# Performance work log

Measured on AMD Instinct MI355X. Metric: run time of the kernel, lower is better.

The kernel has to match this reference:

```python
import jax, jax.numpy as jnp
import numpy as np

N = 30000      # nodes
E = 480000     # edges
K = 32         # subgraph size per node
P = 16384      # contrastive pairs
IN = 1024      # in_dim
H = 512        # hidden
Z = 128        # latent (zdim)
BN = 8         # batch_num
DB = 16        # dec_batch_dim
DEC0 = Z + DB  # decoder input dim after concat with batch embedding


def _ln(x):
    m = jnp.mean(x, axis=-1, keepdims=True)
    v = jnp.var(x, axis=-1, keepdims=True)
    return (x - m) * jax.lax.rsqrt(v + 1e-5)


def _gin(x, src, dst, W, b, norm=True, act=True):
    # GIN aggregation (eps=0): (1+eps)*x + sum_{j in N(i)} x_j, then MLP/linear
    agg = jax.ops.segment_sum(x[src], dst, num_segments=N)
    h = (x + agg) @ W + b
    if norm:
        h = _ln(h)
    if act:
        h = jax.nn.relu(h)
    return h


def _encode(x, src, dst, W0, b0, W1, b1):
    h = _gin(x, src, dst, W0, b0, norm=True, act=True)
    return _gin(h, src, dst, W1, b1, norm=True, act=True)  # last_norm=True


def _decode(z, src, dst, W0, b0, W1, b1):
    h = _gin(z, src, dst, W0, b0, norm=True, act=True)
    return _gin(h, src, dst, W1, b1, norm=False, act=False)  # last_norm=False


def setup_inputs() -> dict:
    key = jax.random.key(0)
    ks = jax.random.split(key, 24)
    s = 0.02
    inp = {
        "x": jax.random.normal(ks[0], (N, IN), jnp.float32),
        "x_shf": jax.random.normal(ks[1], (N, IN), jnp.float32),
        "batch_labels": jax.random.uniform(ks[2], (N, BN), jnp.float32),
        "enc_W0": s * jax.random.normal(ks[3], (IN, H), jnp.float32),
        "enc_b0": jnp.zeros((H,), jnp.float32),
        "enc_W1": s * jax.random.normal(ks[4], (H, Z), jnp.float32),
        "enc_b1": jnp.zeros((Z,), jnp.float32),
        "dec_W0": s * jax.random.normal(ks[5], (DEC0, H), jnp.float32),
        "dec_b0": jnp.zeros((H,), jnp.float32),
        "dec_W1": s * jax.random.normal(ks[6], (H, IN), jnp.float32),
        "dec_b1": jnp.zeros((IN,), jnp.float32),
        "be_W0": s * jax.random.normal(ks[7], (BN, (BN + DB) // 2), jnp.float32),
        "be_b0": jnp.zeros(((BN + DB) // 2,), jnp.float32),
        "be_W1": s * jax.random.normal(ks[8], ((BN + DB) // 2, DB), jnp.float32),
        "be_b1": jnp.zeros((DB,), jnp.float32),
        "bd_W0": s * jax.random.normal(ks[9], (Z, 64), jnp.float32),
        "bd_b0": jnp.zeros((64,), jnp.float32),
        "bd_W1": s * jax.random.normal(ks[10], (64, BN), jnp.float32),
        "bd_b1": jnp.zeros((BN,), jnp.float32),
        "bil_W": s * jax.random.normal(ks[11], (Z, Z), jnp.float32),
        "edge_index": jax.random.randint(ks[12], (2, E), 0, N, jnp.int32),
        "sub_node_idx": jax.random.randint(ks[13], (N, K), 0, N, jnp.int32),
        "positive_ind": jax.random.randint(ks[14], (P,), 0, N, jnp.int32),
        "negative_ind": jax.random.randint(ks[15], (P,), 0, N, jnp.int32),
    }
    return inp


def reference(x, x_shf, batch_labels, enc_W0, enc_b0, enc_W1, enc_b1,
              dec_W0, dec_b0, dec_W1, dec_b1, be_W0, be_b0, be_W1, be_b1,
              bd_W0, bd_b0, bd_W1, bd_b1, bil_W,
              edge_index, sub_node_idx, positive_ind, negative_ind):
    src, dst = edge_index[0], edge_index[1]

    # encoder + subgraph mean pooling (global_mean_pool over fixed-size subgraphs)
    z_node = _encode(x, src, dst, enc_W0, enc_b0, enc_W1, enc_b1)        # [N, Z]
    z_sub = jnp.mean(z_node[sub_node_idx], axis=1)                        # [N, Z]
    z_node_shf = _encode(x_shf, src, dst, enc_W0, enc_b0, enc_W1, enc_b1)
    z_sub_shf = jnp.mean(z_node_shf[sub_node_idx], axis=1)                # [N, Z]

    # batch encoder (MLP, no norm)
    batch_emb = jax.nn.relu(batch_labels @ be_W0 + be_b0) @ be_W1 + be_b1  # [N, DB]

    # bilinear contrastive discriminator
    zp = z_sub[positive_ind]                                              # [P, Z]
    logits_pos = jnp.einsum('pd,de,pe->p', zp, bil_W, z_sub_shf[positive_ind])
    logits_neg = jnp.einsum('pd,de,pe->p', zp, bil_W, z_sub_shf[negative_ind])

    # batch discriminator (MLP)
    logits_batch = jax.nn.relu(z_sub @ bd_W0 + bd_b0) @ bd_W1 + bd_b1     # [N, BN]

    # decoder over node graph with batch embedding concatenated
    z_node_batch = jnp.concatenate([z_node, batch_emb], axis=1)           # [N, Z+DB]
    recon = _decode(z_node_batch, src, dst, dec_W0, dec_b0, dec_W1, dec_b1)  # [N, IN]

    return (z_sub, z_sub_shf, recon, logits_pos, logits_neg, logits_batch)
```

## Files before the change

### kernel.cpp

```cpp
#include <hip/hip_runtime.h>
#include <hip/hip_bf16.h>

#define N_NODES 30000
#define E_EDGES 480000
#define KSUB 32
#define NPAIR 16384

typedef __hip_bfloat16 bf16;
typedef __bf16 bf16x8 __attribute__((ext_vector_type(8)));
typedef float floatx4 __attribute__((ext_vector_type(4)));

static __device__ __forceinline__ unsigned short f2bu(float f) {
    unsigned int u = __float_as_uint(f);
    unsigned int r = (u + 0x7fffu + ((u >> 16) & 1u)) >> 16;
    return (unsigned short)r;
}
static __device__ __forceinline__ float blo(unsigned int u) { return __uint_as_float(u << 16); }
static __device__ __forceinline__ float bhi(unsigned int u) { return __uint_as_float(u & 0xffff0000u); }
static __device__ __forceinline__ unsigned int pk2(float a, float b) {
    return (unsigned int)f2bu(a) | ((unsigned int)f2bu(b) << 16);
}

typedef __attribute__((address_space(1))) const void ga_void;
typedef __attribute__((address_space(3))) void lds_void;
static __device__ __forceinline__ void async16(const void* g, void* l) {
    __builtin_amdgcn_global_load_lds((ga_void*)g, (lds_void*)l, 16, 0, 0);
}

__global__ void transpose_pad(const float* __restrict__ W, int K, int Nd,
                              unsigned short* __restrict__ Wt, int Kpad) {
    int t = blockIdx.x * 256 + threadIdx.x;
    if (t >= Nd * Kpad) return;
    int n = t / Kpad, k = t - n * Kpad;
    Wt[t] = (k < K) ? f2bu(W[(size_t)k * Nd + n]) : (unsigned short)0;
}

__global__ void edge_hist(const int* __restrict__ dst, int* __restrict__ deg) {
    int e = blockIdx.x * 256 + threadIdx.x;
    if (e < E_EDGES) atomicAdd(&deg[dst[e]], 1);
}

__global__ void scan_kernel(const int* __restrict__ deg, int N,
                            int* __restrict__ row_start, int* __restrict__ cursor) {
    __shared__ int sh[1024];
    int t = threadIdx.x;
    int chunk = (N + 1023) >> 10;
    int lo = t * chunk;
    int hi = lo + chunk; if (hi > N) hi = N;
    if (lo > N) lo = N;
    int s = 0;
    for (int i = lo; i < hi; i++) s += deg[i];
    sh[t] = s;
    __syncthreads();
    for (int off = 1; off < 1024; off <<= 1) {
        int v = (t >= off) ? sh[t - off] : 0;
        __syncthreads();
        sh[t] += v;
        __syncthreads();
    }
    int run = (t == 0) ? 0 : sh[t - 1];
    for (int i = lo; i < hi; i++) {
        row_start[i] = run; cursor[i] = run; run += deg[i];
    }
    if (t == 1023) row_start[N] = run;
}

__global__ void edge_scatter(const int* __restrict__ src, const int* __restrict__ dst,
                             int* __restrict__ cursor, int* __restrict__ csr_src) {
    int e = blockIdx.x * 256 + threadIdx.x;
    if (e < E_EDGES) {
        int p = atomicAdd(&cursor[dst[e]], 1);
        if (p >= 0 && p < E_EDGES) csr_src[p] = src[e];
    }
}

template <int D, int DOUT, int DO_LN>
__global__ void csr_agg_ln_h(const unsigned short* __restrict__ X,
                             const int* __restrict__ row_start,
                             const int* __restrict__ csr_src,
                             const float* __restrict__ bias,
                             unsigned short* __restrict__ Y,
                             int addCenter, int doRelu) {
    constexpr int VE = (D % 512 == 0) ? 8 : 2;
    constexpr int R = (D + 64 * VE - 1) / (64 * VE);
    static_assert(VE == 2 || R == 1, "VE8 path assumes single round");
    static_assert(!DO_LN || (D % (64 * VE) == 0), "LN path needs full lanes");
    constexpr int U = D / 2;
    constexpr int UO = DOUT / 2;
    static_assert(D % 2 == 0 && DOUT % 2 == 0, "even dims");

    int node = blockIdx.x * 4 + (threadIdx.x >> 6);
    if (node >= N_NODES) return;
    int lane = threadIdx.x & 63;

    float acc[R][VE];
#pragma unroll
    for (int r = 0; r < R; r++)
#pragma unroll
        for (int i = 0; i < VE; i++) acc[r][i] = 0.0f;

    int s0 = row_start[node], s1 = row_start[node + 1];
    if (s0 < 0) s0 = 0;
    if (s1 > E_EDGES) s1 = E_EDGES;

    if constexpr (VE == 8) {
        auto add_u4 = [&](uint4 u) {
            acc[0][0] += blo(u.x); acc[0][1] += bhi(u.x);
            acc[0][2] += blo(u.y); acc[0][3] += bhi(u.y);
            acc[0][4] += blo(u.z); acc[0][5] += bhi(u.z);
            acc[0][6] += blo(u.w); acc[0][7] += bhi(u.w);
        };
        if (addCenter)
            add_u4(*reinterpret_cast<const uint4*>(X + (size_t)node * D + lane * 8));
        for (int j0 = s0; j0 < s1; j0 += 64) {
            int cnt = s1 - j0; if (cnt > 64) cnt = 64;
            int myi = (lane < cnt) ? csr_src[j0 + lane] : 0;
            int t = 0;
            for (; t + 8 <= cnt; t += 8) {
                uint4 raw[8];
#pragma unroll
                for (int g = 0; g < 8; g++) {
                    int s = __shfl(myi, t + g);
                    if ((unsigned)s >= (unsigned)N_NODES) s = 0;
                    raw[g] = *reinterpret_cast<const uint4*>(X + (size_t)s * D + lane * 8);
                }
#pragma unroll
                for (int g = 0; g < 8; g++) add_u4(raw[g]);
            }
            for (; t < cnt; t++) {
                int s = __shfl(myi, t);
                if ((unsigned)s >= (unsigned)N_NODES) s = 0;
                add_u4(*reinterpret_cast<const uint4*>(X + (size_t)s * D + lane * 8));
            }
        }
        if (bias) {
            const float4* bp = reinterpret_cast<const float4*>(bias + lane * 8);
            float4 b0 = bp[0], b1 = bp[1];
            acc[0][0] += b0.x; acc[0][1] += b0.y; acc[0][2] += b0.z; acc[0][3] += b0.w;
            acc[0][4] += b1.x; acc[0][5] += b1.y; acc[0][6] += b1.z; acc[0][7] += b1.w;
        }
    } else {
        auto add_u = [&](int r, unsigned int u) { acc[r][0] += blo(u); acc[r][1] += bhi(u); };
        if (addCenter) {
#pragma unroll
            for (int r = 0; r < R; r++) {
                int unit = r * 64 + lane;
                if (unit < U)
                    add_u(r, *reinterpret_cast<const unsigned int*>(X + (size_t)node * D + unit * 2));
            }
        }
        for (int j0 = s0; j0 < s1; j0 += 64) {
            int cnt = s1 - j0; if (cnt > 64) cnt = 64;
            int myi = (lane < cnt) ? csr_src[j0 + lane] : 0;
            int t = 0;
            for (; t + 8 <= cnt; t += 8) {
                unsigned int raw[8][R];
#pragma unroll
                for (int g = 0; g < 8; g++) {
                    int s = __shfl(myi, t + g);
                    if ((unsigned)s >= (unsigned)N_NODES) s = 0;
#pragma unroll
                    for (int r = 0; r < R; r++) {
                        int unit = r * 64 + lane;
                        raw[g][r] = (unit < U)
                            ? *reinterpret_cast<const unsigned int*>(X + (size_t)s * D + unit * 2)
                            : 0u;
                    }
                }
#pragma unroll
                for (int g = 0; g < 8; g++)
#pragma unroll
                    for (int r = 0; r < R; r++) add_u(r, raw[g][r]);
            }
            for (; t < cnt; t++) {
                int s = __shfl(myi, t);
                if ((unsigned)s >= (unsigned)N_NODES) s = 0;
#pragma unroll
                for (int r = 0; r < R; r++) {
                    int unit = r * 64 + lane;
                    if (unit < U)
                        add_u(r, *reinterpret_cast<const unsigned int*>(X + (size_t)s * D + unit * 2));
                }
            }
        }
        if (bias) {
#pragma unroll
            for (int r = 0; r < R; r++) {
                int unit = r * 64 + lane;
                if (unit < U) { acc[r][0] += bias[unit * 2]; acc[r][1] += bias[unit * 2 + 1]; }
            }
        }
    }

    if constexpr (DO_LN) {
        float s = 0.0f;
#pragma unroll
        for (int r = 0; r < R; r++)
#pragma unroll
            for (int i = 0; i < VE; i++) s += acc[r][i];
        for (int o = 32; o; o >>= 1) s += __shfl_xor(s, o);
        float mean = s * (1.0f / (float)D);
        float q = 0.0f;
#pragma unroll
        for (int r = 0; r < R; r++)
#pragma unroll
            for (int i = 0; i < VE; i++) { float d = acc[r][i] - mean; q += d * d; }
        for (int o = 32; o; o >>= 1) q += __shfl_xor(q, o);
        float rs_ = rsqrtf(q * (1.0f / (float)D) + 1e-5f);
#pragma unroll
        for (int r = 0; r < R; r++)
#pragma unroll
            for (int i = 0; i < VE; i++) acc[r][i] = (acc[r][i] - mean) * rs_;
    }

    if (doRelu) {
#pragma unroll
        for (int r = 0; r < R; r++)
#pragma unroll
            for (int i = 0; i < VE; i++) if (acc[r][i] < 0.0f) acc[r][i] = 0.0f;
    }

    if constexpr (VE == 8) {
        uint4 o = make_uint4(pk2(acc[0][0], acc[0][1]), pk2(acc[0][2], acc[0][3]),
                             pk2(acc[0][4], acc[0][5]), pk2(acc[0][6], acc[0][7]));
        *reinterpret_cast<uint4*>(Y + (size_t)node * DOUT + lane * 8) = o;
    } else {
        constexpr int RO = (UO + 63) / 64;
#pragma unroll
        for (int r = 0; r < RO; r++) {
            int unit = r * 64 + lane;
            if (unit < UO) {
                unsigned int v = 0u;
                if (r < R && unit < U) v = pk2(acc[r][0], acc[r][1]);
                *reinterpret_cast<unsigned int*>(Y + (size_t)node * DOUT + unit * 2) = v;
            }
        }
    }
}

__global__ void ln_relu_h512(const unsigned short* __restrict__ Yin,
                             const float* __restrict__ bias,
                             unsigned short* __restrict__ Out) {
    int row = blockIdx.x * 4 + (threadIdx.x >> 6);
    if (row >= N_NODES) return;
    int lane = threadIdx.x & 63;
    uint4 u = *reinterpret_cast<const uint4*>(Yin + (size_t)row * 512 + lane * 8);
    const float4* bp = reinterpret_cast<const float4*>(bias + lane * 8);
    float4 b0 = bp[0], b1 = bp[1];
    float v[8];
    v[0] = blo(u.x) + b0.x; v[1] = bhi(u.x) + b0.y;
    v[2] = blo(u.y) + b0.z; v[3] = bhi(u.y) + b0.w;
    v[4] = blo(u.z) + b1.x; v[5] = bhi(u.z) + b1.y;
    v[6] = blo(u.w) + b1.z; v[7] = bhi(u.w) + b1.w;
    float s = 0.0f;
#pragma unroll
    for (int i = 0; i < 8; i++) s += v[i];
    for (int o = 32; o; o >>= 1) s += __shfl_xor(s, o);
    float mean = s * (1.0f / 512.0f);
    float q = 0.0f;
#pragma unroll
    for (int i = 0; i < 8; i++) { float d = v[i] - mean; q += d * d; }
    for (int o = 32; o; o >>= 1) q += __shfl_xor(q, o);
    float rs = rsqrtf(q * (1.0f / 512.0f) + 1e-5f);
#pragma unroll
    for (int i = 0; i < 8; i++) {
        float o = (v[i] - mean) * rs;
        v[i] = o > 0.0f ? o : 0.0f;
    }
    uint4 o = make_uint4(pk2(v[0], v[1]), pk2(v[2], v[3]), pk2(v[4], v[5]), pk2(v[6], v[7]));
    *reinterpret_cast<uint4*>(Out + (size_t)row * 512 + lane * 8) = o;
}

template <int ABF, int CBF, int BLKN>
__global__ __launch_bounds__(BLKN * 2, 2) void gemm_bt(
    const void* __restrict__ A_, int lda, const unsigned short* __restrict__ Bt,
    int M, int K, void* __restrict__ C_, int ldc, const float* __restrict__ bias,
    int nbn) {
    constexpr int THREADS = BLKN * 2;
    constexpr int NW = THREADS / 64;
    constexpr int WNC = BLKN / 64;
    constexpr int ASTR = ABF ? 64 : 72;
    __shared__ __align__(16) unsigned short As[128 * ASTR];
    __shared__ __align__(16) unsigned short Bs[BLKN * 64];

    int lid = blockIdx.x;
    int bmlow = lid & 7;
    int t2 = lid >> 3;
    int bmh = t2 / nbn;
    int bn = t2 - bmh * nbn;
    int bm = bmh * 8 + bmlow;
    if (bm * 128 >= M) return;

    const int t = threadIdx.x;
    const int lane = t & 63;
    const int wave = t >> 6;
    const int wm = wave / WNC, wn = wave % WNC;
    const int quad = lane >> 4, m16 = lane & 15;

    floatx4 acc[4][4];
#pragma unroll
    for (int i = 0; i < 4; i++)
#pragma unroll
        for (int j = 0; j < 4; j++)
#pragma unroll
            for (int r = 0; r < 4; r++) acc[i][j][r] = 0.0f;

    union Pk { unsigned short h[8]; uint4 v; };
    const int l8 = lane >> 3;
    const int gseg = (lane & 7) ^ l8;

    for (int k0 = 0; k0 < K; k0 += 64) {
        if constexpr (ABF) {
            constexpr int ACALLS = 128 / (NW * 8);
#pragma unroll
            for (int i = 0; i < ACALLS; i++) {
                int rb = (i * NW + wave) * 8;
                const unsigned short* gp = (const unsigned short*)A_ +
                    (size_t)(bm * 128 + rb + l8) * lda + k0 + gseg * 8;
                async16(gp, &As[rb * 64]);
            }
        } else {
            constexpr int GR = 1024 / THREADS;
#pragma unroll
            for (int i = 0; i < GR; i++) {
                int q = i * THREADS + t;
                int r = q >> 3, g = q & 7;
                int grow = bm * 128 + r;
                uint4 val = make_uint4(0u, 0u, 0u, 0u);
                if (grow < M) {
                    const float* ap = (const float*)A_ + (size_t)grow * lda + k0 + g * 8;
                    float4 f0 = *reinterpret_cast<const float4*>(ap);
                    float4 f1 = *reinterpret_cast<const float4*>(ap + 4);
                    Pk pk;
                    pk.h[0] = f2bu(f0.x); pk.h[1] = f2bu(f0.y);
                    pk.h[2] = f2bu(f0.z); pk.h[3] = f2bu(f0.w);
                    pk.h[4] = f2bu(f1.x); pk.h[5] = f2bu(f1.y);
                    pk.h[6] = f2bu(f1.z); pk.h[7] = f2bu(f1.w);
                    val = pk.v;
                }
                *reinterpret_cast<uint4*>(&As[r * 72 + g * 8]) = val;
            }
        }
        constexpr int BCALLS = BLKN / (NW * 8);
#pragma unroll
        for (int i = 0; i < BCALLS; i++) {
            int rb = (i * NW + wave) * 8;
            const unsigned short* gp = Bt + (size_t)(bn * BLKN + rb + l8) * K + k0 + gseg * 8;
            async16(gp, &Bs[rb * 64]);
        }
        __syncthreads();
#pragma unroll
        for (int kk = 0; kk < 2; kk++) {
            bf16x8 af[4], bfr[4];
#pragma unroll
            for (int i = 0; i < 4; i++) {
                int r = wm * 64 + i * 16 + m16;
                int off;
                if constexpr (ABF) off = r * 64 + (((kk * 4 + quad) ^ (r & 7)) * 8);
                else off = r * 72 + (kk * 4 + quad) * 8;
                af[i] = *reinterpret_cast<const bf16x8*>(&As[off]);
            }
#pragma unroll
            for (int j = 0; j < 4; j++) {
                int r = wn * 64 + j * 16 + m16;
                bfr[j] = *reinterpret_cast<const bf16x8*>(&Bs[r * 64 + (((kk * 4 + quad) ^ (r & 7)) * 8)]);
            }
#pragma unroll
            for (int i = 0; i < 4; i++)
#pragma unroll
                for (int j = 0; j < 4; j++)
                    acc[i][j] = __builtin_amdgcn_mfma_f32_16x16x32_bf16(af[i], bfr[j], acc[i][j], 0, 0, 0);
        }
        __syncthreads();
    }
#pragma unroll
    for (int i = 0; i < 4; i++) {
        int r0 = bm * 128 + wm * 64 + i * 16 + quad * 4;
#pragma unroll
        for (int j = 0; j < 4; j++) {
            int c = bn * BLKN + wn * 64 + j * 16 + m16;
            float bia = bias ? bias[c] : 0.0f;
#pragma unroll
            for (int r = 0; r < 4; r++) {
                int row = r0 + r;
                if (row < M) {
                    float val = acc[i][j][r] + bia;
                    if constexpr (CBF)
                        ((unsigned short*)C_)[(size_t)row * ldc + c] = f2bu(val);
                    else
                        ((float*)C_)[(size_t)row * ldc + c] = val;
                }
            }
        }
    }
}

__global__ void pool_kernel_h(const unsigned short* __restrict__ zn, const int* __restrict__ idx,
                              float* __restrict__ out) {
    int i = blockIdx.x * 4 + (threadIdx.x >> 6);
    if (i >= N_NODES) return;
    int lane = threadIdx.x & 63;
    int myi = (lane < KSUB) ? idx[i * KSUB + lane] : 0;
    float ax = 0.0f, ay = 0.0f;
#pragma unroll
    for (int t = 0; t < KSUB; t++) {
        int s = __shfl(myi, t);
        if ((unsigned)s >= (unsigned)N_NODES) s = 0;
        unsigned int u = *reinterpret_cast<const unsigned int*>(zn + (size_t)s * 128 + lane * 2);
        ax += blo(u); ay += bhi(u);
    }
    *reinterpret_cast<float2*>(out + (size_t)i * 128 + lane * 2) =
        make_float2(ax * (1.0f / KSUB), ay * (1.0f / KSUB));
}

__global__ void batch_emb_kernel(const float* __restrict__ bl, const float* __restrict__ W0,
                                 const float* __restrict__ b0, const float* __restrict__ W1,
                                 const float* __restrict__ b1, float* __restrict__ out) {
    int i = blockIdx.x * 256 + threadIdx.x;
    if (i >= N_NODES) return;
    float in[8];
#pragma unroll
    for (int d = 0; d < 8; d++) in[d] = bl[(size_t)i * 8 + d];
    float h[12];
#pragma unroll
    for (int j = 0; j < 12; j++) {
        float a = b0[j];
#pragma unroll
        for (int d = 0; d < 8; d++) a += in[d] * W0[d * 12 + j];
        h[j] = a > 0.0f ? a : 0.0f;
    }
#pragma unroll
    for (int j = 0; j < 16; j++) {
        float a = b1[j];
#pragma unroll
        for (int k = 0; k < 12; k++) a += h[k] * W1[k * 16 + j];
        out[(size_t)i * 16 + j] = a;
    }
}

__global__ void concat_kernel_h(const unsigned short* __restrict__ zn,
                                const float* __restrict__ be,
                                unsigned short* __restrict__ znb) {
    int i = blockIdx.x;
    int t = threadIdx.x;
    if (t < 128) znb[(size_t)i * 144 + t] = zn[(size_t)i * 128 + t];
    else if (t < 144) znb[(size_t)i * 144 + t] = f2bu(be[(size_t)i * 16 + (t - 128)]);
}

__global__ void bilinear_dot(const float* __restrict__ U, const float* __restrict__ z_shf,
                             const int* __restrict__ pos, const int* __restrict__ neg,
                             float* __restrict__ out_pos, float* __restrict__ out_neg) {
    int p = blockIdx.x * 4 + (threadIdx.x >> 6);
    if (p >= NPAIR) return;
    int lane = threadIdx.x & 63;
    int ip = pos[p], in_ = neg[p];
    if ((unsigned)ip >= (unsigned)N_NODES) ip = 0;
    if ((unsigned)in_ >= (unsigned)N_NODES) in_ = 0;
    float2 u = *reinterpret_cast<const float2*>(U + (size_t)ip * 128 + lane * 2);
    float2 zp = *reinterpret_cast<const float2*>(z_shf + (size_t)ip * 128 + lane * 2);
    float2 zn = *reinterpret_cast<const float2*>(z_shf + (size_t)in_ * 128 + lane * 2);
    float vp = u.x * zp.x + u.y * zp.y;
    float vn = u.x * zn.x + u.y * zn.y;
    for (int o = 32; o; o >>= 1) { vp += __shfl_xor(vp, o); vn += __shfl_xor(vn, o); }
    if (lane == 0) { out_pos[p] = vp; out_neg[p] = vn; }
}

__global__ void bd_kernel(const float* __restrict__ z_sub, const float* __restrict__ W0,
                          const float* __restrict__ b0, const float* __restrict__ W1,
                          const float* __restrict__ b1, float* __restrict__ out) {
    __shared__ float zsh[4][128];
    __shared__ float hsh[4][64];
    int w = threadIdx.x >> 6, lane = threadIdx.x & 63;
    int node = blockIdx.x * 4 + w;
    zsh[w][lane] = z_sub[(size_t)node * 128 + lane];
    zsh[w][64 + lane] = z_sub[(size_t)node * 128 + 64 + lane];
    __syncthreads();
    float h = b0[lane];
    for (int d = 0; d < 128; d++) h += zsh[w][d] * W0[d * 64 + lane];
    if (h < 0.0f) h = 0.0f;
    hsh[w][lane] = h;
    __syncthreads();
    if (lane < 8) {
        float o = b1[lane];
        for (int l = 0; l < 64; l++) o += hsh[w][l] * W1[l * 8 + lane];
        out[(size_t)node * 8 + lane] = o;
    }
}

extern "C" void kernel_launch(void* const* d_in, const int* in_sizes, int n_in,
                              void* d_out, int out_size, void* d_ws, size_t ws_size,
                              hipStream_t stream) {
    const float* x = (const float*)d_in[0];
    const float* x_shf = (const float*)d_in[1];
    const float* blab = (const float*)d_in[2];
    const float* encW0 = (const float*)d_in[3];
    const float* encb0 = (const float*)d_in[4];
    const float* encW1 = (const float*)d_in[5];
    const float* encb1 = (const float*)d_in[6];
    const float* decW0 = (const float*)d_in[7];
    const float* decb0 = (const float*)d_in[8];
    const float* decW1 = (const float*)d_in[9];
    const float* decb1 = (const float*)d_in[10];
    const float* beW0 = (const float*)d_in[11];
    const float* beb0 = (const float*)d_in[12];
    const float* beW1 = (const float*)d_in[13];
    const float* beb1 = (const float*)d_in[14];
    const float* bdW0 = (const float*)d_in[15];
    const float* bdb0 = (const float*)d_in[16];
    const float* bdW1 = (const float*)d_in[17];
    const float* bdb1 = (const float*)d_in[18];
    const float* bilW = (const float*)d_in[19];
    const int* eidx = (const int*)d_in[20];
    const int* subidx = (const int*)d_in[21];
    const int* posi = (const int*)d_in[22];
    const int* negi = (const int*)d_in[23];
    float* out = (float*)d_out;

    char* ws = (char*)d_ws;
    size_t off = 0;
    auto alloc = [&](size_t bytes) -> void* {
        void* p = ws + off;
        off += (bytes + 255) & ~(size_t)255;
        return p;
    };
    unsigned short* encW0t = (unsigned short*)alloc((size_t)512 * 1024 * 2);
    unsigned short* encW1t = (unsigned short*)alloc((size_t)128 * 512 * 2);
    unsigned short* decW0t = (unsigned short*)alloc((size_t)512 * 192 * 2);
    unsigned short* decW1t = (unsigned short*)alloc((size_t)1024 * 512 * 2);
    unsigned short* bilWt = (unsigned short*)alloc((size_t)128 * 128 * 2);
    int* deg = (int*)alloc((size_t)N_NODES * 4);
    int* row_start = (int*)alloc((size_t)(N_NODES + 1) * 4);
    int* cursor = (int*)alloc((size_t)N_NODES * 4);
    int* csr_src = (int*)alloc((size_t)E_EDGES * 4);
    unsigned short* y0h = (unsigned short*)alloc((size_t)N_NODES * 512 * 2);
    unsigned short* agg0h = (unsigned short*)alloc((size_t)N_NODES * 512 * 2);
    unsigned short* y1h = (unsigned short*)alloc((size_t)N_NODES * 128 * 2);
    unsigned short* znh = (unsigned short*)alloc((size_t)N_NODES * 128 * 2);
    unsigned short* znsh = (unsigned short*)alloc((size_t)N_NODES * 128 * 2);
    unsigned short* znbh = (unsigned short*)alloc((size_t)N_NODES * 144 * 2);
    unsigned short* s1h = (unsigned short*)alloc((size_t)N_NODES * 192 * 2);
    float* bembf = (float*)alloc((size_t)N_NODES * 16 * 4);
    float* Ubil = (float*)alloc((size_t)N_NODES * 128 * 4);
    alloc(262144);
    if (off > ws_size) return;

    const int* e_src = eidx;
    const int* e_dst = eidx + E_EDGES;

    transpose_pad<<<(512 * 1024 + 255) / 256, 256, 0, stream>>>(encW0, 1024, 512, encW0t, 1024);
    transpose_pad<<<(128 * 512 + 255) / 256, 256, 0, stream>>>(encW1, 512, 128, encW1t, 512);
    transpose_pad<<<(512 * 192 + 255) / 256, 256, 0, stream>>>(decW0, 144, 512, decW0t, 192);
    transpose_pad<<<(1024 * 512 + 255) / 256, 256, 0, stream>>>(decW1, 512, 1024, decW1t, 512);
    transpose_pad<<<(128 * 128 + 255) / 256, 256, 0, stream>>>(bilW, 128, 128, bilWt, 128);

    hipMemsetAsync(deg, 0, (size_t)N_NODES * 4, stream);
    edge_hist<<<E_EDGES / 256, 256, 0, stream>>>(e_dst, deg);
    scan_kernel<<<1, 1024, 0, stream>>>(deg, N_NODES, row_start, cursor);
    edge_scatter<<<E_EDGES / 256, 256, 0, stream>>>(e_src, e_dst, cursor, csr_src);

    for (int pass = 0; pass < 2; pass++) {
        const float* xin = pass ? x_shf : x;
        unsigned short* zn = pass ? znsh : znh;
        float* zsub_out = out + (pass ? 3840000 : 0);
        gemm_bt<0, 1, 256><<<480, 512, 0, stream>>>(xin, 1024, encW0t, N_NODES, 1024, y0h, 512, nullptr, 2);
        csr_agg_ln_h<512, 512, 1><<<7500, 256, 0, stream>>>(y0h, row_start, csr_src, encb0, agg0h, 1, 1);
        gemm_bt<1, 1, 128><<<240, 256, 0, stream>>>(agg0h, 512, encW1t, N_NODES, 512, y1h, 128, nullptr, 1);
        csr_agg_ln_h<128, 128, 1><<<7500, 256, 0, stream>>>(y1h, row_start, csr_src, encb1, zn, 1, 1);
        pool_kernel_h<<<7500, 256, 0, stream>>>(zn, subidx, zsub_out);
    }

    batch_emb_kernel<<<(N_NODES + 255) / 256, 256, 0, stream>>>(blab, beW0, beb0, beW1, beb1, bembf);
    concat_kernel_h<<<30000, 192, 0, stream>>>(znh, bembf, znbh);

    csr_agg_ln_h<144, 192, 0><<<7500, 256, 0, stream>>>(znbh, row_start, csr_src, nullptr, s1h, 1, 0);
    gemm_bt<1, 1, 256><<<480, 512, 0, stream>>>(s1h, 192, decW0t, N_NODES, 192, y0h, 512, nullptr, 2);
    ln_relu_h512<<<7500, 256, 0, stream>>>(y0h, decb0, y0h);
    csr_agg_ln_h<512, 512, 0><<<7500, 256, 0, stream>>>(y0h, row_start, csr_src, nullptr, agg0h, 1, 0);
    gemm_bt<1, 0, 256><<<960, 512, 0, stream>>>(agg0h, 512, decW1t, N_NODES, 512, out + 7680000, 1024, decb1, 4);

    gemm_bt<0, 0, 128><<<240, 256, 0, stream>>>(out, 128, bilWt, N_NODES, 128, Ubil, 128, nullptr, 1);
    bilinear_dot<<<(NPAIR + 3) / 4, 256, 0, stream>>>(Ubil, out + 3840000, posi, negi,
                                                      out + 38400000, out + 38416384);
    bd_kernel<<<7500, 256, 0, stream>>>(out, bdW0, bdb0, bdW1, bdb1, out + 38432768);
}
```

Before: 1.060 ms.

## Batch both encoder passes, fuse concat into decoder aggregation, double-buffer gathers

Runs the original and shuffled encoder passes together: their outputs go into stacked 60000-row buffers so each aggregation, the second GEMM and the pooling launch once over both. The five weight transposes become a single kernel, and the concat kernel is removed by a dedicated decoder aggregation that reads z and the batch embedding directly. The D=512 gather loop is software-pipelined with two 8-row register buffers, the narrow path gathers 16 rows per batch, and launch bounds are added. The aim is to cut launch count, fill the GPU better, and keep more memory loads in flight, at the cost of higher register pressure and more complex indexing.

Measured after the change: 1.015 ms. 4.3% less time.

```diff
diff --git a/kernel.cpp b/kernel.cpp
--- a/kernel.cpp
+++ b/kernel.cpp
@@ -27,12 +27,22 @@
     __builtin_amdgcn_global_load_lds((ga_void*)g, (lds_void*)l, 16, 0, 0);
 }
 
-__global__ void transpose_pad(const float* __restrict__ W, int K, int Nd,
-                              unsigned short* __restrict__ Wt, int Kpad) {
+__global__ void transpose_all(const float* __restrict__ encW0, const float* __restrict__ encW1,
+                              const float* __restrict__ decW0, const float* __restrict__ decW1,
+                              const float* __restrict__ bilW,
+                              unsigned short* __restrict__ encW0t, unsigned short* __restrict__ encW1t,
+                              unsigned short* __restrict__ decW0t, unsigned short* __restrict__ decW1t,
+                              unsigned short* __restrict__ bilWt) {
     int t = blockIdx.x * 256 + threadIdx.x;
-    if (t >= Nd * Kpad) return;
-    int n = t / Kpad, k = t - n * Kpad;
-    Wt[t] = (k < K) ? f2bu(W[(size_t)k * Nd + n]) : (unsigned short)0;
+    const float* W; unsigned short* Wt; int K, Nd, Kpad, u;
+    if (t < 524288) { W = encW0; Wt = encW0t; K = 1024; Nd = 512; Kpad = 1024; u = t; }
+    else if (t < 589824) { W = encW1; Wt = encW1t; K = 512; Nd = 128; Kpad = 512; u = t - 524288; }
+    else if (t < 688128) { W = decW0; Wt = decW0t; K = 144; Nd = 512; Kpad = 192; u = t - 589824; }
+    else if (t < 1212416) { W = decW1; Wt = decW1t; K = 512; Nd = 1024; Kpad = 512; u = t - 688128; }
+    else if (t < 1228800) { W = bilW; Wt = bilWt; K = 128; Nd = 128; Kpad = 128; u = t - 1212416; }
+    else return;
+    int n = u / Kpad, k = u - n * Kpad;
+    Wt[u] = (k < K) ? f2bu(W[(size_t)k * Nd + n]) : (unsigned short)0;
 }
 
 __global__ void edge_hist(const int* __restrict__ dst, int* __restrict__ deg) {
@@ -75,23 +85,21 @@
 }
 
 template <int D, int DOUT, int DO_LN>
-__global__ void csr_agg_ln_h(const unsigned short* __restrict__ X,
-                             const int* __restrict__ row_start,
-                             const int* __restrict__ csr_src,
-                             const float* __restrict__ bias,
-                             unsigned short* __restrict__ Y,
-                             int addCenter, int doRelu) {
+__global__ __launch_bounds__(256, 4) void csr_agg_ln_h(
+    const unsigned short* __restrict__ Xa, const unsigned short* __restrict__ Xb, int nv,
+    const int* __restrict__ row_start, const int* __restrict__ csr_src,
+    const float* __restrict__ bias, unsigned short* __restrict__ Y,
+    int addCenter, int doRelu) {
     constexpr int VE = (D % 512 == 0) ? 8 : 2;
     constexpr int R = (D + 64 * VE - 1) / (64 * VE);
     static_assert(VE == 2 || R == 1, "VE8 path assumes single round");
-    static_assert(!DO_LN || (D % (64 * VE) == 0), "LN path needs full lanes");
-    constexpr int U = D / 2;
-    constexpr int UO = DOUT / 2;
-    static_assert(D % 2 == 0 && DOUT % 2 == 0, "even dims");
-
-    int node = blockIdx.x * 4 + (threadIdx.x >> 6);
-    if (node >= N_NODES) return;
+    static_assert(D % (64 * VE) == 0 && D == DOUT, "paths need exact divisibility");
+
+    int v = blockIdx.x * 4 + (threadIdx.x >> 6);
+    if (v >= nv) return;
     int lane = threadIdx.x & 63;
+    const unsigned short* X = (v < N_NODES) ? Xa : Xb;
+    int node = (v < N_NODES) ? v : v - N_NODES;
 
     float acc[R][VE];
 #pragma unroll
@@ -115,22 +123,32 @@
         for (int j0 = s0; j0 < s1; j0 += 64) {
             int cnt = s1 - j0; if (cnt > 64) cnt = 64;
             int myi = (lane < cnt) ? csr_src[j0 + lane] : 0;
-            int t = 0;
-            for (; t + 8 <= cnt; t += 8) {
-                uint4 raw[8];
+            uint4 rawA[8], rawB[8];
+            auto issue8 = [&](uint4 (&raw)[8], int tb) {
 #pragma unroll
                 for (int g = 0; g < 8; g++) {
-                    int s = __shfl(myi, t + g);
+                    int s = __shfl(myi, (tb + g) & 63);
                     if ((unsigned)s >= (unsigned)N_NODES) s = 0;
                     raw[g] = *reinterpret_cast<const uint4*>(X + (size_t)s * D + lane * 8);
                 }
-#pragma unroll
-                for (int g = 0; g < 8; g++) add_u4(raw[g]);
-            }
-            for (; t < cnt; t++) {
-                int s = __shfl(myi, t);
-                if ((unsigned)s >= (unsigned)N_NODES) s = 0;
-                add_u4(*reinterpret_cast<const uint4*>(X + (size_t)s * D + lane * 8));
+            };
+            auto consume8 = [&](uint4 (&raw)[8], int tb) {
+#pragma unroll
+                for (int g = 0; g < 8; g++)
+                    if (tb + g < cnt) add_u4(raw[g]);
+            };
+            issue8(rawA, 0);
+            int t = 0;
+            while (true) {
+                if (t + 8 < cnt) {
+                    issue8(rawB, t + 8);
+                    consume8(rawA, t);
+                    if (t + 16 < cnt) {
+                        issue8(rawA, t + 16);
+                        consume8(rawB, t + 8);
+                        t += 16;
+                    } else { consume8(rawB, t + 8); break; }
+                } else { consume8(rawA, t); break; }
             }
         }
         if (bias) {
@@ -143,51 +161,34 @@
         auto add_u = [&](int r, unsigned int u) { acc[r][0] += blo(u); acc[r][1] += bhi(u); };
         if (addCenter) {
 #pragma unroll
-            for (int r = 0; r < R; r++) {
-                int unit = r * 64 + lane;
-                if (unit < U)
-                    add_u(r, *reinterpret_cast<const unsigned int*>(X + (size_t)node * D + unit * 2));
-            }
+            for (int r = 0; r < R; r++)
+                add_u(r, *reinterpret_cast<const unsigned int*>(X + (size_t)node * D + (r * 64 + lane) * 2));
         }
         for (int j0 = s0; j0 < s1; j0 += 64) {
             int cnt = s1 - j0; if (cnt > 64) cnt = 64;
             int myi = (lane < cnt) ? csr_src[j0 + lane] : 0;
-            int t = 0;
-            for (; t + 8 <= cnt; t += 8) {
-                unsigned int raw[8][R];
-#pragma unroll
-                for (int g = 0; g < 8; g++) {
-                    int s = __shfl(myi, t + g);
+            for (int t = 0; t < cnt; t += 16) {
+                unsigned int raw[16][R];
+#pragma unroll
+                for (int g = 0; g < 16; g++) {
+                    int s = __shfl(myi, (t + g) & 63);
                     if ((unsigned)s >= (unsigned)N_NODES) s = 0;
 #pragma unroll
-                    for (int r = 0; r < R; r++) {
-                        int unit = r * 64 + lane;
-                        raw[g][r] = (unit < U)
-                            ? *reinterpret_cast<const unsigned int*>(X + (size_t)s * D + unit * 2)
-                            : 0u;
-                    }
+                    for (int r = 0; r < R; r++)
+                        raw[g][r] = *reinterpret_cast<const unsigned int*>(X + (size_t)s * D + (r * 64 + lane) * 2);
                 }
 #pragma unroll
-                for (int g = 0; g < 8; g++)
-#pragma unroll
-                    for (int r = 0; r < R; r++) add_u(r, raw[g][r]);
-            }
-            for (; t < cnt; t++) {
-                int s = __shfl(myi, t);
-                if ((unsigned)s >= (unsigned)N_NODES) s = 0;
-#pragma unroll
-                for (int r = 0; r < R; r++) {
-                    int unit = r * 64 + lane;
-                    if (unit < U)
-                        add_u(r, *reinterpret_cast<const unsigned int*>(X + (size_t)s * D + unit * 2));
-                }
+                for (int g = 0; g < 16; g++)
+                    if (t + g < cnt)
+#pragma unroll
+                        for (int r = 0; r < R; r++) add_u(r, raw[g][r]);
             }
         }
         if (bias) {
 #pragma unroll
             for (int r = 0; r < R; r++) {
                 int unit = r * 64 + lane;
-                if (unit < U) { acc[r][0] += bias[unit * 2]; acc[r][1] += bias[unit * 2 + 1]; }
+                acc[r][0] += bias[unit * 2]; acc[r][1] += bias[unit * 2 + 1];
             }
         }
     }
@@ -223,19 +224,64 @@
     if constexpr (VE == 8) {
         uint4 o = make_uint4(pk2(acc[0][0], acc[0][1]), pk2(acc[0][2], acc[0][3]),
                              pk2(acc[0][4], acc[0][5]), pk2(acc[0][6], acc[0][7]));
-        *reinterpret_cast<uint4*>(Y + (size_t)node * DOUT + lane * 8) = o;
+        *reinterpret_cast<uint4*>(Y + (size_t)v * DOUT + lane * 8) = o;
     } else {
-        constexpr int RO = (UO + 63) / 64;
-#pragma unroll
-        for (int r = 0; r < RO; r++) {
-            int unit = r * 64 + lane;
-            if (unit < UO) {
-                unsigned int v = 0u;
-                if (r < R && unit < U) v = pk2(acc[r][0], acc[r][1]);
-                *reinterpret_cast<unsigned int*>(Y + (size_t)node * DOUT + unit * 2) = v;
-            }
-        }
-    }
+#pragma unroll
+        for (int r = 0; r < R; r++)
+            *reinterpret_cast<unsigned int*>(Y + (size_t)v * DOUT + (r * 64 + lane) * 2) =
+                pk2(acc[r][0], acc[r][1]);
+    }
+}
+
+__global__ __launch_bounds__(256, 4) void csr_agg_dec(
+    const unsigned short* __restrict__ zn, const float* __restrict__ be,
+    const int* __restrict__ row_start, const int* __restrict__ csr_src,
+    unsigned short* __restrict__ Y) {
+    int node = blockIdx.x * 4 + (threadIdx.x >> 6);
+    if (node >= N_NODES) return;
+    int lane = threadIdx.x & 63;
+    float az0 = 0.0f, az1 = 0.0f, ab0 = 0.0f, ab1 = 0.0f;
+    {
+        unsigned int u = *reinterpret_cast<const unsigned int*>(zn + (size_t)node * 128 + lane * 2);
+        az0 += blo(u); az1 += bhi(u);
+        if (lane < 8) {
+            float2 b = *reinterpret_cast<const float2*>(be + (size_t)node * 16 + lane * 2);
+            ab0 += b.x; ab1 += b.y;
+        }
+    }
+    int s0 = row_start[node], s1 = row_start[node + 1];
+    if (s0 < 0) s0 = 0;
+    if (s1 > E_EDGES) s1 = E_EDGES;
+    for (int j0 = s0; j0 < s1; j0 += 64) {
+        int cnt = s1 - j0; if (cnt > 64) cnt = 64;
+        int myi = (lane < cnt) ? csr_src[j0 + lane] : 0;
+        for (int t = 0; t < cnt; t += 8) {
+            unsigned int rawZ[8]; float2 rawB[8];
+            int sv[8];
+#pragma unroll
+            for (int g = 0; g < 8; g++) {
+                int s = __shfl(myi, (t + g) & 63);
+                if ((unsigned)s >= (unsigned)N_NODES) s = 0;
+                sv[g] = s;
+                rawZ[g] = *reinterpret_cast<const unsigned int*>(zn + (size_t)s * 128 + lane * 2);
+            }
+            if (lane < 8) {
+#pragma unroll
+                for (int g = 0; g < 8; g++)
+                    rawB[g] = *reinterpret_cast<const float2*>(be + (size_t)sv[g] * 16 + lane * 2);
+            }
+#pragma unroll
+            for (int g = 0; g < 8; g++) {
+                if (t + g < cnt) {
+                    az0 += blo(rawZ[g]); az1 += bhi(rawZ[g]);
+                    if (lane < 8) { ab0 += rawB[g].x; ab1 += rawB[g].y; }
+                }
+            }
+        }
+    }
+    unsigned int* yr = reinterpret_cast<unsigned int*>(Y + (size_t)node * 192);
+    yr[lane] = pk2(az0, az1);
+    if (lane < 32) yr[64 + lane] = (lane < 8) ? pk2(ab0, ab1) : 0u;
 }
 
 __global__ void ln_relu_h512(const unsigned short* __restrict__ Yin,
@@ -397,20 +443,23 @@
 
 __global__ void pool_kernel_h(const unsigned short* __restrict__ zn, const int* __restrict__ idx,
                               float* __restrict__ out) {
-    int i = blockIdx.x * 4 + (threadIdx.x >> 6);
-    if (i >= N_NODES) return;
+    int v = blockIdx.x * 4 + (threadIdx.x >> 6);
+    if (v >= 2 * N_NODES) return;
     int lane = threadIdx.x & 63;
+    int pass = v >= N_NODES;
+    int i = pass ? v - N_NODES : v;
+    int roff = pass ? N_NODES : 0;
     int myi = (lane < KSUB) ? idx[i * KSUB + lane] : 0;
     float ax = 0.0f, ay = 0.0f;
 #pragma unroll
     for (int t = 0; t < KSUB; t++) {
         int s = __shfl(myi, t);
         if ((unsigned)s >= (unsigned)N_NODES) s = 0;
-        unsigned int u = *reinterpret_cast<const unsigned int*>(zn + (size_t)s * 128 + lane * 2);
+        unsigned int u = *reinterpret_cast<const unsigned int*>(zn + (size_t)(s + roff) * 128 + lane * 2);
         ax += blo(u); ay += bhi(u);
     }
-    *reinterpret_cast<float2*>(out + (size_t)i * 128 + lane * 2) =
-        make_float2(ax * (1.0f / KSUB), ay * (1.0f / KSUB));
+    float* op = out + (pass ? 3840000 : 0) + (size_t)i * 128 + lane * 2;
+    *reinterpret_cast<float2*>(op) = make_float2(ax * (1.0f / KSUB), ay * (1.0f / KSUB));
 }
 
 __global__ void batch_emb_kernel(const float* __restrict__ bl, const float* __restrict__ W0,
@@ -436,15 +485,6 @@
         for (int k = 0; k < 12; k++) a += h[k] * W1[k * 16 + j];
         out[(size_t)i * 16 + j] = a;
     }
-}
-
-__global__ void concat_kernel_h(const unsigned short* __restrict__ zn,
-                                const float* __restrict__ be,
-                                unsigned short* __restrict__ znb) {
-    int i = blockIdx.x;
-    int t = threadIdx.x;
-    if (t < 128) znb[(size_t)i * 144 + t] = zn[(size_t)i * 128 + t];
-    else if (t < 144) znb[(size_t)i * 144 + t] = f2bu(be[(size_t)i * 16 + (t - 128)]);
 }
 
 __global__ void bilinear_dot(const float* __restrict__ U, const float* __restrict__ z_shf,
@@ -532,12 +572,10 @@
     int* row_start = (int*)alloc((size_t)(N_NODES + 1) * 4);
     int* cursor = (int*)alloc((size_t)N_NODES * 4);
     int* csr_src = (int*)alloc((size_t)E_EDGES * 4);
-    unsigned short* y0h = (unsigned short*)alloc((size_t)N_NODES * 512 * 2);
-    unsigned short* agg0h = (unsigned short*)alloc((size_t)N_NODES * 512 * 2);
-    unsigned short* y1h = (unsigned short*)alloc((size_t)N_NODES * 128 * 2);
-    unsigned short* znh = (unsigned short*)alloc((size_t)N_NODES * 128 * 2);
-    unsigned short* znsh = (unsigned short*)alloc((size_t)N_NODES * 128 * 2);
-    unsigned short* znbh = (unsigned short*)alloc((size_t)N_NODES * 144 * 2);
+    unsigned short* y0h = (unsigned short*)alloc((size_t)60000 * 512 * 2);
+    unsigned short* agg0h = (unsigned short*)alloc((size_t)60000 * 512 * 2);
+    unsigned short* y1h = (unsigned short*)alloc((size_t)60000 * 128 * 2);
+    unsigned short* znh = (unsigned short*)alloc((size_t)60000 * 128 * 2);
     unsigned short* s1h = (unsigned short*)alloc((size_t)N_NODES * 192 * 2);
     float* bembf = (float*)alloc((size_t)N_NODES * 16 * 4);
     float* Ubil = (float*)alloc((size_t)N_NODES * 128 * 4);
@@ -547,35 +585,30 @@
     const int* e_src = eidx;
     const int* e_dst = eidx + E_EDGES;
 
-    transpose_pad<<<(512 * 1024 + 255) / 256, 256, 0, stream>>>(encW0, 1024, 512, encW0t, 1024);
-    transpose_pad<<<(128 * 512 + 255) / 256, 256, 0, stream>>>(encW1, 512, 128, encW1t, 512);
-    transpose_pad<<<(512 * 192 + 255) / 256, 256, 0, stream>>>(decW0, 144, 512, decW0t, 192);
-    transpose_pad<<<(1024 * 512 + 255) / 256, 256, 0, stream>>>(decW1, 512, 1024, decW1t, 512);
-    transpose_pad<<<(128 * 128 + 255) / 256, 256, 0, stream>>>(bilW, 128, 128, bilWt, 128);
+    transpose_all<<<4800, 256, 0, stream>>>(encW0, encW1, decW0, decW1, bilW,
+                                            encW0t, encW1t, decW0t, decW1t, bilWt);
 
     hipMemsetAsync(deg, 0, (size_t)N_NODES * 4, stream);
     edge_hist<<<E_EDGES / 256, 256, 0, stream>>>(e_dst, deg);
     scan_kernel<<<1, 1024, 0, stream>>>(deg, N_NODES, row_start, cursor);
     edge_scatter<<<E_EDGES / 256, 256, 0, stream>>>(e_src, e_dst, cursor, csr_src);
 
-    for (int pass = 0; pass < 2; pass++) {
-        const float* xin = pass ? x_shf : x;
-        unsigned short* zn = pass ? znsh : znh;
-        float* zsub_out = out + (pass ? 3840000 : 0);
-        gemm_bt<0, 1, 256><<<480, 512, 0, stream>>>(xin, 1024, encW0t, N_NODES, 1024, y0h, 512, nullptr, 2);
-        csr_agg_ln_h<512, 512, 1><<<7500, 256, 0, stream>>>(y0h, row_start, csr_src, encb0, agg0h, 1, 1);
-        gemm_bt<1, 1, 128><<<240, 256, 0, stream>>>(agg0h, 512, encW1t, N_NODES, 512, y1h, 128, nullptr, 1);
-        csr_agg_ln_h<128, 128, 1><<<7500, 256, 0, stream>>>(y1h, row_start, csr_src, encb1, zn, 1, 1);
-        pool_kernel_h<<<7500, 256, 0, stream>>>(zn, subidx, zsub_out);
-    }
+    unsigned short* y0b = y0h + (size_t)N_NODES * 512;
+    unsigned short* y1b = y1h + (size_t)N_NODES * 128;
+
+    gemm_bt<0, 1, 256><<<480, 512, 0, stream>>>(x, 1024, encW0t, N_NODES, 1024, y0h, 512, nullptr, 2);
+    gemm_bt<0, 1, 256><<<480, 512, 0, stream>>>(x_shf, 1024, encW0t, N_NODES, 1024, y0b, 512, nullptr, 2);
+    csr_agg_ln_h<512, 512, 1><<<15000, 256, 0, stream>>>(y0h, y0b, 60000, row_start, csr_src, encb0, agg0h, 1, 1);
+    gemm_bt<1, 1, 128><<<472, 256, 0, stream>>>(agg0h, 512, encW1t, 60000, 512, y1h, 128, nullptr, 1);
+    csr_agg_ln_h<128, 128, 1><<<15000, 256, 0, stream>>>(y1h, y1b, 60000, row_start, csr_src, encb1, znh, 1, 1);
+    pool_kernel_h<<<15000, 256, 0, stream>>>(znh, subidx, out);
 
     batch_emb_kernel<<<(N_NODES + 255) / 256, 256, 0, stream>>>(blab, beW0, beb0, beW1, beb1, bembf);
-    concat_kernel_h<<<30000, 192, 0, stream>>>(znh, bembf, znbh);
-
-    csr_agg_ln_h<144, 192, 0><<<7500, 256, 0, stream>>>(znbh, row_start, csr_src, nullptr, s1h, 1, 0);
+    csr_agg_dec<<<7500, 256, 0, stream>>>(znh, bembf, row_start, csr_src, s1h);
+
     gemm_bt<1, 1, 256><<<480, 512, 0, stream>>>(s1h, 192, decW0t, N_NODES, 192, y0h, 512, nullptr, 2);
     ln_relu_h512<<<7500, 256, 0, stream>>>(y0h, decb0, y0h);
-    csr_agg_ln_h<512, 512, 0><<<7500, 256, 0, stream>>>(y0h, row_start, csr_src, nullptr, agg0h, 1, 0);
+    csr_agg_ln_h<512, 512, 0><<<7500, 256, 0, stream>>>(y0h, y0h, N_NODES, row_start, csr_src, nullptr, agg0h, 1, 0);
     gemm_bt<1, 0, 256><<<960, 512, 0, stream>>>(agg0h, 512, decW1t, N_NODES, 512, out + 7680000, 1024, decb1, 4);
 
     gemm_bt<0, 0, 128><<<240, 256, 0, stream>>>(out, 128, bilWt, N_NODES, 128, Ubil, 128, nullptr, 1);
```
